# Kernel optimization log

Measured on AMD Instinct MI355X. Metric: run time of the kernel, lower is better.

## Reference

```python
import jax, jax.numpy as jnp
import numpy as np

D_K = 8192   # sequence length (module calls it d_k)
D_MODEL = 128

def setup_inputs() -> dict:
    key = jax.random.key(0)
    k1, k2, k3 = jax.random.split(key, 3)
    Q = jax.random.normal(k1, (D_K, D_MODEL), dtype=jnp.float32)
    K = jax.random.normal(k2, (D_K, D_MODEL), dtype=jnp.float32)
    V = jax.random.normal(k3, (D_K, D_MODEL), dtype=jnp.float32)
    return {"Q": Q, "K": K, "V": V}

def reference(Q, K, V):
    # scores: [d_k, d_k] -- full attention matrix, scaled by 1/sqrt(d_k)
    # (faithful to the source: scale uses d_k, the sequence dim)
    inv_scale = 1.0 / jnp.sqrt(jnp.asarray(D_K, dtype=Q.dtype))
    scores = jnp.einsum('qd,kd->qk', Q, K) * inv_scale
    attn = jax.nn.softmax(scores, axis=-1)
    return jnp.einsum('qk,kd->qd', attn, V)
```

## Files before the change

kernel.cpp:

```cpp
#include <hip/hip_runtime.h>

#define SEQ 8192
#define DM  128
#define KS  8

typedef __attribute__((ext_vector_type(8)))  short bf16x8;
typedef __attribute__((ext_vector_type(16))) float f32x16;

static __device__ __forceinline__ unsigned short f2bf(float f) {
    unsigned int u = __builtin_bit_cast(unsigned int, f);
    u += 0x7FFFu + ((u >> 16) & 1u);
    return (unsigned short)(u >> 16);
}
static __device__ __forceinline__ unsigned int pack2bf(float a, float b) {
    return ((unsigned int)f2bf(b) << 16) | (unsigned int)f2bf(a);
}
static __device__ __forceinline__ float bflo(unsigned int u) {
    return __builtin_bit_cast(float, u << 16);
}
static __device__ __forceinline__ float bfhi(unsigned int u) {
    return __builtin_bit_cast(float, u & 0xFFFF0000u);
}
static __device__ __forceinline__ bf16x8 as_frag(uint4 v) {
    return __builtin_bit_cast(bf16x8, v);
}
static __device__ __forceinline__ unsigned int pack2bf_trunc(float a, float b) {
    return __builtin_amdgcn_perm(__builtin_bit_cast(unsigned int, b),
                                 __builtin_bit_cast(unsigned int, a), 0x07060302u);
}
static __device__ __forceinline__ void gl_lds16(const void* g, void* l) {
    __builtin_amdgcn_global_load_lds(
        (const __attribute__((address_space(1))) void*)(unsigned long long)g,
        (__attribute__((address_space(3))) void*)(unsigned int)(unsigned long long)l,
        16, 0, 0);
}
#define CL2 (1.4426950408889634f / 90.50966799187809f)

__global__ __launch_bounds__(512) void prep_kernel(
        const float* __restrict__ Q, const float* __restrict__ K,
        const float* __restrict__ V,
        uint2* __restrict__ Qb2, uint4* __restrict__ Kt, uint4* __restrict__ Vt) {
    __shared__ float VL[32 * 132 + 4];
    const int b = blockIdx.x, tid = threadIdx.x;
    const float4* Q4 = (const float4*)Q;
    const float4* K4 = (const float4*)K;
    const float4* V4 = (const float4*)V;

    #pragma unroll
    for (int u = 0; u < 2; ++u) {
        int f4 = u * 512 + tid;
        int k = f4 >> 5, c4 = f4 & 31;
        float4 v = V4[(size_t)b * 1024 + f4];
        *(float4*)(VL + k * 132 + c4 * 4) = v;
    }
    #pragma unroll
    for (int u = 0; u < 2; ++u) {
        int f4 = u * 512 + tid;
        float4 v = Q4[(size_t)b * 1024 + f4];
        Qb2[(size_t)b * 1024 + f4] = make_uint2(pack2bf(v.x * CL2, v.y * CL2),
                                                pack2bf(v.z * CL2, v.w * CL2));
    }
    {
        int p = tid;
        int q = p & 31, h = (p >> 5) & 1, s = p >> 6;
        int fi = (b * 32 + q) * 32 + s * 4 + h * 2;
        float4 a = K4[fi], c = K4[fi + 1];
        Kt[(size_t)b * 512 + p] = make_uint4(pack2bf(a.x, a.y), pack2bf(a.z, a.w),
                                             pack2bf(c.x, c.y), pack2bf(c.z, c.w));
    }
    __syncthreads();
    {
        int p = tid;
        int q = p & 31, h = (p >> 5) & 1, w = p >> 6;
        int d = (w >> 1) * 32 + q;
        int k0 = (w & 1) * 16 + h * 8;
        unsigned int r[4];
        #pragma unroll
        for (int jj = 0; jj < 4; ++jj) {
            float e0 = VL[(k0 + 2 * jj) * 132 + d];
            float e1 = VL[(k0 + 2 * jj + 1) * 132 + d];
            r[jj] = pack2bf(e0, e1);
        }
        Vt[(size_t)b * 512 + p] = make_uint4(r[0], r[1], r[2], r[3]);
    }
}

__global__ __launch_bounds__(512, 2) void attn_kernel(
        const unsigned short* __restrict__ Qb,
        const uint4* __restrict__ Kt,
        const uint4* __restrict__ Vt,
        uint2* __restrict__ Opart, float* __restrict__ Lpart) {
    __shared__ __align__(16) char smem[65536];
    __shared__ float Lx[128];
    const int tid = threadIdx.x;
    const int wid = tid >> 6, lane = tid & 63;
    const int i = wid & 3, j = wid >> 2;
    const int q = lane & 31, h = lane >> 5;
    const int qt = blockIdx.x & 63, ks = blockIdx.x >> 6;
    const int qbase = qt * 128 + i * 32;
    const int tile0 = ks * 32 + j * 16;

    uint4 qf[8];
    {
        const unsigned short* qrow = Qb + (qbase + q) * DM + 8 * h;
        #pragma unroll
        for (int s = 0; s < 8; ++s) qf[s] = *(const uint4*)(qrow + 16 * s);
    }

    f32x16 oacc[4];
    #pragma unroll
    for (int mb = 0; mb < 4; ++mb)
        #pragma unroll
        for (int r = 0; r < 16; ++r) oacc[mb][r] = 0.f;
    float lsum = 0.f;

    char* const mybuf = smem + j * 32768;
    auto stage = [&](int buf, int tile) {
        char* base = mybuf + buf * 16384;
        const uint4* kt = Kt + (size_t)tile * 512;
        const uint4* vt = Vt + (size_t)tile * 512;
        #pragma unroll
        for (int u = 0; u < 2; ++u) {
            int ki = i * 2 + u;
            gl_lds16(kt + ki * 64 + lane, base + ki * 1024);
            gl_lds16(vt + ki * 64 + lane, base + 8192 + ki * 1024);
        }
    };

    stage(0, tile0);
    #pragma unroll 1
    for (int t = 0; t < 16; ++t) {
        __syncthreads();
        if (t < 15) stage((t + 1) & 1, tile0 + t + 1);
        const char* kl = mybuf + (t & 1) * 16384 + lane * 16;

        uint4 kf[8];
        #pragma unroll
        for (int s = 0; s < 8; ++s) kf[s] = *(const uint4*)(kl + s * 1024);

        f32x16 sacc;
        #pragma unroll
        for (int r = 0; r < 16; ++r) sacc[r] = 0.f;
        __builtin_amdgcn_s_setprio(1);
        #pragma unroll
        for (int s = 0; s < 8; ++s)
            sacc = __builtin_amdgcn_mfma_f32_32x32x16_bf16(
                       as_frag(kf[s]), as_frag(qf[s]), sacc, 0, 0, 0);
        __builtin_amdgcn_s_setprio(0);

        uint4 vf[8];
        #pragma unroll
        for (int w = 0; w < 8; ++w) vf[w] = *(const uint4*)(kl + 8192 + w * 1024);

        float p[16];
        #pragma unroll
        for (int r = 0; r < 16; ++r) {
            p[r] = __builtin_amdgcn_exp2f(sacc[r]);
            lsum += p[r];
        }
        unsigned int pk[8], px[8];
        #pragma unroll
        for (int jj = 0; jj < 8; ++jj) pk[jj] = pack2bf_trunc(p[2 * jj], p[2 * jj + 1]);
        #pragma unroll
        for (int jj = 0; jj < 8; ++jj) px[jj] = (unsigned int)__shfl_xor((int)pk[jj], 32);
        uint4 B0, B1;
        B0.x = h ? px[2] : pk[0];  B0.y = h ? px[3] : pk[1];
        B0.z = h ? pk[2] : px[0];  B0.w = h ? pk[3] : px[1];
        B1.x = h ? px[6] : pk[4];  B1.y = h ? px[7] : pk[5];
        B1.z = h ? pk[6] : px[4];  B1.w = h ? pk[7] : px[5];

        __builtin_amdgcn_s_setprio(1);
        #pragma unroll
        for (int mb = 0; mb < 4; ++mb) {
            oacc[mb] = __builtin_amdgcn_mfma_f32_32x32x16_bf16(
                           as_frag(vf[mb * 2 + 0]), as_frag(B0), oacc[mb], 0, 0, 0);
            oacc[mb] = __builtin_amdgcn_mfma_f32_32x32x16_bf16(
                           as_frag(vf[mb * 2 + 1]), as_frag(B1), oacc[mb], 0, 0, 0);
        }
        __builtin_amdgcn_s_setprio(0);
    }

    float l2 = lsum + __shfl_xor(lsum, 32);
    __syncthreads();
    float* Lg = (float*)(smem + i * 16384);
    if (j == 0) {
        #pragma unroll
        for (int mb = 0; mb < 4; ++mb)
            #pragma unroll
            for (int r = 0; r < 16; ++r) {
                int dl = 32 * mb + (r & 3) + 8 * (r >> 2) + 4 * h;
                Lg[dl * 32 + q] = oacc[mb][r];
            }
        if (h == 0) Lx[i * 32 + q] = l2;
    }
    __syncthreads();
    if (j == 1) {
        #pragma unroll
        for (int mb = 0; mb < 4; ++mb)
            #pragma unroll
            for (int r = 0; r < 16; ++r) {
                int dl = 32 * mb + (r & 3) + 8 * (r >> 2) + 4 * h;
                Lg[dl * 32 + q] += oacc[mb][r];
            }
        if (h == 0) Lpart[(size_t)ks * SEQ + qbase + q] = Lx[i * 32 + q] + l2;
    }
    __syncthreads();
    #pragma unroll
    for (int u = 0; u < 8; ++u) {
        int idx = u * 512 + tid;
        int rd = idx >> 5, c4 = idx & 31;
        int ig = c4 >> 3, q4 = c4 & 7;
        float4 v = *(const float4*)(smem + ig * 16384 + (rd * 8 + q4) * 16);
        Opart[(((size_t)(ks * 64 + qt)) * 128 + rd) * 32 + c4] =
            make_uint2(pack2bf(v.x, v.y), pack2bf(v.z, v.w));
    }
}

__global__ __launch_bounds__(512) void reduce_kernel(
        const uint2* __restrict__ Opart, const float* __restrict__ Lpart,
        float* __restrict__ Out) {
    __shared__ float T[32 * 132 + 4];
    __shared__ float Rinv[128];
    const int tid = threadIdx.x;
    const int qt = blockIdx.x & 63, dq = blockIdx.x >> 6;
    if (tid < 128) {
        float L = 0.f;
        #pragma unroll
        for (int ks = 0; ks < KS; ++ks) L += Lpart[(size_t)ks * SEQ + qt * 128 + tid];
        Rinv[tid] = 1.0f / L;
    }
    const int c = tid & 31, dsub = tid >> 5;
    float4 acc[2];
    #pragma unroll
    for (int rr = 0; rr < 2; ++rr) { acc[rr].x = acc[rr].y = acc[rr].z = acc[rr].w = 0.f; }
    #pragma unroll
    for (int ks = 0; ks < KS; ++ks) {
        #pragma unroll
        for (int rr = 0; rr < 2; ++rr) {
            int d_l = rr * 16 + dsub;
            uint2 w = Opart[(((size_t)(ks * 64 + qt)) * 128 + dq * 32 + d_l) * 32 + c];
            acc[rr].x += bflo(w.x); acc[rr].y += bfhi(w.x);
            acc[rr].z += bflo(w.y); acc[rr].w += bfhi(w.y);
        }
    }
    #pragma unroll
    for (int rr = 0; rr < 2; ++rr)
        *(float4*)(T + (rr * 16 + dsub) * 132 + c * 4) = acc[rr];
    __syncthreads();
    const int q_l = tid >> 2, part = tid & 3;
    float r = Rinv[q_l];
    #pragma unroll
    for (int g = 0; g < 2; ++g) {
        int d0 = part * 8 + g * 4;
        float4 o;
        o.x = T[(d0 + 0) * 132 + q_l] * r;
        o.y = T[(d0 + 1) * 132 + q_l] * r;
        o.z = T[(d0 + 2) * 132 + q_l] * r;
        o.w = T[(d0 + 3) * 132 + q_l] * r;
        *(float4*)(Out + ((size_t)(qt * 128 + q_l)) * DM + dq * 32 + d0) = o;
    }
}

extern "C" void kernel_launch(void* const* d_in, const int* in_sizes, int n_in,
                              void* d_out, int out_size, void* d_ws, size_t ws_size,
                              hipStream_t stream) {
    const float* Q = (const float*)d_in[0];
    const float* K = (const float*)d_in[1];
    const float* V = (const float*)d_in[2];
    char* ws = (char*)d_ws;
    uint2* Qb2  = (uint2*)ws;
    uint4* Kt   = (uint4*)(ws + 2 * 1024 * 1024);
    uint4* Vt   = (uint4*)(ws + 4 * 1024 * 1024);
    float* Lpart= (float*)(ws + 6 * 1024 * 1024);
    uint2* Opart= (uint2*)(ws + 6 * 1024 * 1024 + 262144);
    float* Out  = (float*)d_out;

    prep_kernel<<<256, 512, 0, stream>>>(Q, K, V, Qb2, Kt, Vt);
    attn_kernel<<<512, 512, 0, stream>>>((const unsigned short*)Qb2, Kt, Vt,
                                         Opart, Lpart);
    reduce_kernel<<<256, 512, 0, stream>>>(Opart, Lpart, Out);
}
```

Baseline: 113.2 us.

## Load V directly to registers, use permlane32_swap, split row-sum accumulators

V tiles are no longer staged through LDS. Each wave reads its V fragments straight from global memory into registers at the top of the iteration, which halves the LDS buffer footprint and the LDS traffic. The cross-half shuffle of the bf16 probabilities is replaced by four permlane32_swap intrinsics instead of eight shfl_xor plus selects. The softmax denominator is accumulated in four independent partial sums to shorten the dependency chain. The risk is global load latency for V being exposed, since nothing prefetches it a tile ahead.

```diff
diff --git a/kernel.cpp b/kernel.cpp
--- a/kernel.cpp
+++ b/kernel.cpp
@@ -6,6 +6,7 @@
 
 typedef __attribute__((ext_vector_type(8)))  short bf16x8;
 typedef __attribute__((ext_vector_type(16))) float f32x16;
+typedef __attribute__((ext_vector_type(2)))  unsigned int uintx2;
 
 static __device__ __forceinline__ unsigned short f2bf(float f) {
     unsigned int u = __builtin_bit_cast(unsigned int, f);
@@ -112,18 +113,16 @@
     for (int mb = 0; mb < 4; ++mb)
         #pragma unroll
         for (int r = 0; r < 16; ++r) oacc[mb][r] = 0.f;
-    float lsum = 0.f;
-
-    char* const mybuf = smem + j * 32768;
+    float ls0 = 0.f, ls1 = 0.f, ls2 = 0.f, ls3 = 0.f;
+
+    char* const mybuf = smem + j * 16384;
     auto stage = [&](int buf, int tile) {
-        char* base = mybuf + buf * 16384;
+        char* base = mybuf + buf * 8192;
         const uint4* kt = Kt + (size_t)tile * 512;
-        const uint4* vt = Vt + (size_t)tile * 512;
         #pragma unroll
         for (int u = 0; u < 2; ++u) {
             int ki = i * 2 + u;
             gl_lds16(kt + ki * 64 + lane, base + ki * 1024);
-            gl_lds16(vt + ki * 64 + lane, base + 8192 + ki * 1024);
         }
     };
 
@@ -131,8 +130,14 @@
     #pragma unroll 1
     for (int t = 0; t < 16; ++t) {
         __syncthreads();
+        uint4 vf[8];
+        {
+            const uint4* vt = Vt + (size_t)(tile0 + t) * 512 + lane;
+            #pragma unroll
+            for (int w = 0; w < 8; ++w) vf[w] = vt[w * 64];
+        }
         if (t < 15) stage((t + 1) & 1, tile0 + t + 1);
-        const char* kl = mybuf + (t & 1) * 16384 + lane * 16;
+        const char* kl = mybuf + (t & 1) * 8192 + lane * 16;
 
         uint4 kf[8];
         #pragma unroll
@@ -148,26 +153,28 @@
                        as_frag(kf[s]), as_frag(qf[s]), sacc, 0, 0, 0);
         __builtin_amdgcn_s_setprio(0);
 
-        uint4 vf[8];
-        #pragma unroll
-        for (int w = 0; w < 8; ++w) vf[w] = *(const uint4*)(kl + 8192 + w * 1024);
-
         float p[16];
         #pragma unroll
-        for (int r = 0; r < 16; ++r) {
-            p[r] = __builtin_amdgcn_exp2f(sacc[r]);
-            lsum += p[r];
-        }
-        unsigned int pk[8], px[8];
+        for (int r = 0; r < 16; ++r) p[r] = __builtin_amdgcn_exp2f(sacc[r]);
+        #pragma unroll
+        for (int r = 0; r < 4; ++r) {
+            ls0 += p[4 * r + 0]; ls1 += p[4 * r + 1];
+            ls2 += p[4 * r + 2]; ls3 += p[4 * r + 3];
+        }
+        unsigned int pk[8];
         #pragma unroll
         for (int jj = 0; jj < 8; ++jj) pk[jj] = pack2bf_trunc(p[2 * jj], p[2 * jj + 1]);
-        #pragma unroll
-        for (int jj = 0; jj < 8; ++jj) px[jj] = (unsigned int)__shfl_xor((int)pk[jj], 32);
         uint4 B0, B1;
-        B0.x = h ? px[2] : pk[0];  B0.y = h ? px[3] : pk[1];
-        B0.z = h ? pk[2] : px[0];  B0.w = h ? pk[3] : px[1];
-        B1.x = h ? px[6] : pk[4];  B1.y = h ? px[7] : pk[5];
-        B1.z = h ? pk[6] : px[4];  B1.w = h ? pk[7] : px[5];
+        {
+            uintx2 r0 = __builtin_amdgcn_permlane32_swap(pk[0], pk[2], false, false);
+            uintx2 r1 = __builtin_amdgcn_permlane32_swap(pk[1], pk[3], false, false);
+            uintx2 r4 = __builtin_amdgcn_permlane32_swap(pk[4], pk[6], false, false);
+            uintx2 r5 = __builtin_amdgcn_permlane32_swap(pk[5], pk[7], false, false);
+            B0.x = r0[0];  B0.z = r0[1];
+            B0.y = r1[0];  B0.w = r1[1];
+            B1.x = r4[0];  B1.z = r4[1];
+            B1.y = r5[0];  B1.w = r5[1];
+        }
 
         __builtin_amdgcn_s_setprio(1);
         #pragma unroll
@@ -179,6 +186,7 @@
         }
         __builtin_amdgcn_s_setprio(0);
     }
+    float lsum = (ls0 + ls1) + (ls2 + ls3);
 
     float l2 = lsum + __shfl_xor(lsum, 32);
     __syncthreads();
```

Result: no change. 114.3 us (+1.0%).
